# Optimization experiments

Measured on AMD Instinct MI355X. Metric: run time of the kernel, lower is better.

The kernel has to match this reference:

```python
import jax, jax.numpy as jnp
import numpy as np

B, S, H, NH = 2, 2048, 2048, 16
HD = H // NH

def setup_inputs() -> dict:
    key = jax.random.key(0)
    ks = jax.random.split(key, 6)
    scale = 1.0 / np.sqrt(H)
    return {
        "x": jax.random.normal(ks[0], (B, S, H), dtype=jnp.float32),
        "Wq": jax.random.normal(ks[1], (H, H), dtype=jnp.float32) * scale,
        "Wk": jax.random.normal(ks[2], (H, H), dtype=jnp.float32) * scale,
        "Wv": jax.random.normal(ks[3], (H, H), dtype=jnp.float32) * scale,
        "Wo": jax.random.normal(ks[4], (H, H), dtype=jnp.float32) * scale,
        "bo": jax.random.normal(ks[5], (H,), dtype=jnp.float32) * 0.01,
    }

def reference(x, Wq, Wk, Wv, Wo, bo):
    # nn.Linear convention: y = x @ W.T (W is [out, in])
    q = (x @ Wq.T).reshape(B, S, NH, HD).transpose(0, 2, 1, 3)  # [B,NH,S,HD]
    k = (x @ Wk.T).reshape(B, S, NH, HD).transpose(0, 2, 1, 3)
    v = (x @ Wv.T).reshape(B, S, NH, HD).transpose(0, 2, 1, 3)
    scale = jnp.asarray(HD, x.dtype) ** -0.5
    scores = jnp.einsum('bhqd,bhkd->bhqk', q, k) * scale  # [B,NH,S,S]
    attn = jax.nn.softmax(scores, axis=-1)
    out = jnp.einsum('bhqk,bhkd->bhqd', attn, v)  # [B,NH,S,HD]
    out = out.transpose(0, 2, 1, 3).reshape(B, S, H)
    return out @ Wo.T + bo
```

## Files before the change

### kernel.cpp

```cpp
#include <hip/hip_runtime.h>
#include <hip/hip_bf16.h>
#include <stdint.h>

#define S_LEN 2048
#define NHEADS 16
#define HDIM 128
#define H_TOT 2048
#define BATCH 2
#define M_TOK 4096
#define KDIM 2048

typedef __attribute__((ext_vector_type(8))) short bf16x8;
typedef __attribute__((ext_vector_type(4))) float f32x4;
typedef __attribute__((ext_vector_type(16))) float f32x16;

__device__ inline ushort bf16rn(float f) {
  union { float f; uint32_t u; } x; x.f = f;
  uint32_t r = x.u + 0x7FFF + ((x.u >> 16) & 1);
  return (ushort)(r >> 16);
}

__global__ __launch_bounds__(256) void cvt_bf16_kernel(const float* __restrict__ in,
                                                       ushort* __restrict__ out, int n4) {
  int i = blockIdx.x * blockDim.x + threadIdx.x;
  int stride = gridDim.x * blockDim.x;
  for (; i < n4; i += stride) {
    float4 v = reinterpret_cast<const float4*>(in)[i];
    ushort4 o;
    o.x = bf16rn(v.x); o.y = bf16rn(v.y); o.z = bf16rn(v.z); o.w = bf16rn(v.w);
    reinterpret_cast<ushort4*>(out)[i] = o;
  }
}

template<int MODE>
__global__ __launch_bounds__(256) void gemm_nt(const ushort* __restrict__ A,
                                               const ushort* __restrict__ Bw,
                                               void* __restrict__ Cout,
                                               const float* __restrict__ bias,
                                               float scale) {
  __shared__ ushort As[128 * 32];
  __shared__ ushort Bs[128 * 32];
  const int K = KDIM;
  int tid = threadIdx.x;
  int wave = tid >> 6, lane = tid & 63;
  int bm = blockIdx.y * 128, bn = blockIdx.x * 128;
  int wr = wave >> 1, wc = wave & 1;

  f32x4 acc[4][4];
#pragma unroll
  for (int i = 0; i < 4; i++)
#pragma unroll
    for (int j = 0; j < 4; j++) acc[i][j] = (f32x4){0.f, 0.f, 0.f, 0.f};

  int r0 = wave * 32 + (lane >> 2);
  int c8 = (lane & 3) * 8;
  const ushort* gA0 = A + (size_t)(bm + r0) * K + c8;
  const ushort* gA1 = gA0 + 16 * (size_t)K;
  const ushort* gB0 = Bw + (size_t)(bn + r0) * K + c8;
  const ushort* gB1 = gB0 + 16 * (size_t)K;
  ushort* lA0 = As + (wave * 2 + 0) * 512;
  ushort* lA1 = As + (wave * 2 + 1) * 512;
  ushort* lB0 = Bs + (wave * 2 + 0) * 512;
  ushort* lB1 = Bs + (wave * 2 + 1) * 512;

  int aoff = (wr * 64 + (lane & 15)) * 32 + (lane >> 4) * 8;
  int boff = (wc * 64 + (lane & 15)) * 32 + (lane >> 4) * 8;

  for (int kt = 0; kt < K; kt += 32) {
    __builtin_amdgcn_global_load_lds((const __attribute__((address_space(1))) void*)gA0,
                                     (__attribute__((address_space(3))) void*)lA0, 16, 0, 0);
    __builtin_amdgcn_global_load_lds((const __attribute__((address_space(1))) void*)gA1,
                                     (__attribute__((address_space(3))) void*)lA1, 16, 0, 0);
    __builtin_amdgcn_global_load_lds((const __attribute__((address_space(1))) void*)gB0,
                                     (__attribute__((address_space(3))) void*)lB0, 16, 0, 0);
    __builtin_amdgcn_global_load_lds((const __attribute__((address_space(1))) void*)gB1,
                                     (__attribute__((address_space(3))) void*)lB1, 16, 0, 0);
    __syncthreads();

    bf16x8 af[4], bfm[4];
#pragma unroll
    for (int i = 0; i < 4; i++) af[i] = *reinterpret_cast<const bf16x8*>(&As[aoff + i * 512]);
#pragma unroll
    for (int j = 0; j < 4; j++) bfm[j] = *reinterpret_cast<const bf16x8*>(&Bs[boff + j * 512]);
#pragma unroll
    for (int i = 0; i < 4; i++)
#pragma unroll
      for (int j = 0; j < 4; j++)
        acc[i][j] = __builtin_amdgcn_mfma_f32_16x16x32_bf16(af[i], bfm[j], acc[i][j], 0, 0, 0);
    __syncthreads();

    gA0 += 32; gA1 += 32; gB0 += 32; gB1 += 32;
  }

  int rbase = bm + wr * 64 + (lane >> 4) * 4;
  int cbase = bn + wc * 64 + (lane & 15);
  if (MODE == 2) {
    float* Cf = (float*)Cout;
#pragma unroll
    for (int j = 0; j < 4; j++) {
      int n = cbase + j * 16;
      float bv = bias[n];
#pragma unroll
      for (int i = 0; i < 4; i++)
#pragma unroll
        for (int q = 0; q < 4; q++) {
          int m = rbase + i * 16 + q;
          Cf[(size_t)m * H_TOT + n] = acc[i][j][q] + bv;
        }
    }
  } else {
    ushort* Cb = (ushort*)Cout;
#pragma unroll
    for (int j = 0; j < 4; j++) {
      int n = cbase + j * 16;
      int h = n >> 7, d = n & 127;
#pragma unroll
      for (int i = 0; i < 4; i++)
#pragma unroll
        for (int q = 0; q < 4; q++) {
          int m = rbase + i * 16 + q;
          int b = m >> 11, s = m & 2047;
          int bh = b * NHEADS + h;
          size_t idx;
          if (MODE == 0) {
            idx = (((size_t)(bh * 64 + (s >> 5)) * 8 + (d >> 4)) * 64 +
                   ((d >> 3) & 1) * 32 + (s & 31)) * 8 + (d & 7);
          } else {
            int r = s & 15;
            int e = (r & 3) | ((r >> 1) & 4);
            int hi = (r >> 2) & 1;
            idx = (((size_t)(bh * 64 + (s >> 5)) * 8 + ((s >> 4) & 1) * 4 + (d >> 5)) * 64 +
                   hi * 32 + (d & 31)) * 8 + e;
          }
          Cb[idx] = bf16rn(acc[i][j][q] * scale);
        }
    }
  }
}

__global__ __launch_bounds__(256) void attn_kernel(const ushort* __restrict__ Qf,
                                                   const ushort* __restrict__ Kf,
                                                   const ushort* __restrict__ Vf,
                                                   ushort* __restrict__ Ob) {
  __shared__ __attribute__((aligned(16))) ushort KV[2][8192];
  __shared__ float lsinv[4][32];
  int lane = threadIdx.x & 63, wave = threadIdx.x >> 6;
  int hi = lane >> 5;

  int bid = blockIdx.x;
  int swz = (bid & 7) * 64 + (bid >> 3);
  int bh = swz >> 4, qt = swz & 15;
  int b = bh >> 4, h = bh & 15;
  int qrow0 = qt * 128 + wave * 32;

  const bf16x8* Qv = reinterpret_cast<const bf16x8*>(Qf) +
                     ((size_t)(bh * 64 + qt * 4 + wave) * 8) * 64 + lane;
  bf16x8 qf[8];
#pragma unroll
  for (int kc = 0; kc < 8; kc++) qf[kc] = Qv[kc * 64];

  f32x16 oacc[4];
#pragma unroll
  for (int d32 = 0; d32 < 4; d32++)
#pragma unroll
    for (int r = 0; r < 16; r++) oacc[d32][r] = 0.f;
  float lsum = 0.f;

  const ushort* Kbase = Kf;
  const ushort* Vbase = Vf;
  int laneoff = lane * 8;

#define STAGE(kt, bufsel)                                                                  \
  {                                                                                        \
    size_t gchunk = ((size_t)(bh * 64 + (kt))) * 8;                                        \
    _Pragma("unroll")                                                                      \
    for (int i = 0; i < 4; i++) {                                                          \
      int cc = wave * 4 + i;                                                               \
      const ushort* src = (cc < 8) ? (Kbase + (gchunk + cc) * 512 + laneoff)               \
                                   : (Vbase + (gchunk + (cc - 8)) * 512 + laneoff);        \
      __builtin_amdgcn_global_load_lds((const __attribute__((address_space(1))) void*)src, \
                                       (__attribute__((address_space(3))) void*)           \
                                           (&KV[bufsel][cc * 512]),                        \
                                       16, 0, 0);                                          \
    }                                                                                      \
  }

  STAGE(0, 0);
  asm volatile("s_waitcnt vmcnt(0)" ::: "memory");
  __syncthreads();

  const int NT = S_LEN / 32;
  for (int t = 0; t < NT; t++) {
    if (t + 1 < NT) STAGE(t + 1, (t + 1) & 1);
    const ushort* lb = &KV[t & 1][0];

    f32x16 S;
#pragma unroll
    for (int r = 0; r < 16; r++) S[r] = 0.f;
    __builtin_amdgcn_s_setprio(1);
#pragma unroll
    for (int kc = 0; kc < 8; kc++) {
      bf16x8 kfr = *reinterpret_cast<const bf16x8*>(&lb[kc * 512 + laneoff]);
      S = __builtin_amdgcn_mfma_f32_32x32x16_bf16(kfr, qf[kc], S, 0, 0, 0);
    }
    __builtin_amdgcn_s_setprio(0);

    float p[16];
#pragma unroll
    for (int r = 0; r < 16; r++) {
      p[r] = exp2f(S[r]);
      lsum += p[r];
    }
    union { bf16x8 v; uint32_t u[4]; } pa0, pa1;
#pragma unroll
    for (int j = 0; j < 4; j++) {
      uint32_t w0, w1;
      asm("v_cvt_pk_bf16_f32 %0, %1, %2" : "=v"(w0) : "v"(p[2 * j]), "v"(p[2 * j + 1]));
      asm("v_cvt_pk_bf16_f32 %0, %1, %2" : "=v"(w1) : "v"(p[8 + 2 * j]), "v"(p[9 + 2 * j]));
      pa0.u[j] = w0;
      pa1.u[j] = w1;
    }

    __builtin_amdgcn_s_setprio(1);
#pragma unroll
    for (int d32 = 0; d32 < 4; d32++) {
      bf16x8 v0 = *reinterpret_cast<const bf16x8*>(&lb[4096 + (0 + d32) * 512 + laneoff]);
      bf16x8 v1 = *reinterpret_cast<const bf16x8*>(&lb[4096 + (4 + d32) * 512 + laneoff]);
      oacc[d32] = __builtin_amdgcn_mfma_f32_32x32x16_bf16(pa0.v, v0, oacc[d32], 0, 0, 0);
      oacc[d32] = __builtin_amdgcn_mfma_f32_32x32x16_bf16(pa1.v, v1, oacc[d32], 0, 0, 0);
    }
    __builtin_amdgcn_s_setprio(0);

    asm volatile("s_waitcnt vmcnt(0)" ::: "memory");
    __syncthreads();
  }

  float total = lsum + __shfl_xor(lsum, 32);
  if (lane < 32) lsinv[wave][lane] = 1.0f / total;
  __syncthreads();

  float ls[16];
#pragma unroll
  for (int r = 0; r < 16; r++) ls[r] = lsinv[wave][(r & 3) + 8 * (r >> 2) + 4 * hi];
#pragma unroll
  for (int d32 = 0; d32 < 4; d32++)
#pragma unroll
    for (int r = 0; r < 16; r++) {
      int row = (r & 3) + 8 * (r >> 2) + 4 * hi;
      size_t idx = ((size_t)(b * S_LEN + qrow0 + row)) * H_TOT + h * HDIM + d32 * 32 + (lane & 31);
      Ob[idx] = bf16rn(oacc[d32][r] * ls[r]);
    }
#undef STAGE
}

extern "C" void kernel_launch(void* const* d_in, const int* in_sizes, int n_in,
                              void* d_out, int out_size, void* d_ws, size_t ws_size,
                              hipStream_t stream) {
  const float* x  = (const float*)d_in[0];
  const float* Wq = (const float*)d_in[1];
  const float* Wk = (const float*)d_in[2];
  const float* Wv = (const float*)d_in[3];
  const float* Wo = (const float*)d_in[4];
  const float* bo = (const float*)d_in[5];
  float* out = (float*)d_out;

  char* w = (char*)d_ws;
  ushort* xb  = (ushort*)w; w += (size_t)M_TOK * KDIM * 2;
  ushort* Wqb = (ushort*)w; w += (size_t)KDIM * KDIM * 2;
  ushort* Wkb = (ushort*)w; w += (size_t)KDIM * KDIM * 2;
  ushort* Wvb = (ushort*)w; w += (size_t)KDIM * KDIM * 2;
  ushort* Wob = (ushort*)w; w += (size_t)KDIM * KDIM * 2;
  ushort* Qh  = (ushort*)w; w += (size_t)M_TOK * KDIM * 2;
  ushort* Kh  = (ushort*)w; w += (size_t)M_TOK * KDIM * 2;
  ushort* Vt  = (ushort*)w; w += (size_t)M_TOK * KDIM * 2;
  ushort* Ob  = (ushort*)w; w += (size_t)M_TOK * KDIM * 2;

  hipLaunchKernelGGL(cvt_bf16_kernel, dim3(2048), dim3(256), 0, stream, x,  xb,  M_TOK * KDIM / 4);
  hipLaunchKernelGGL(cvt_bf16_kernel, dim3(1024), dim3(256), 0, stream, Wq, Wqb, KDIM * KDIM / 4);
  hipLaunchKernelGGL(cvt_bf16_kernel, dim3(1024), dim3(256), 0, stream, Wk, Wkb, KDIM * KDIM / 4);
  hipLaunchKernelGGL(cvt_bf16_kernel, dim3(1024), dim3(256), 0, stream, Wv, Wvb, KDIM * KDIM / 4);
  hipLaunchKernelGGL(cvt_bf16_kernel, dim3(1024), dim3(256), 0, stream, Wo, Wob, KDIM * KDIM / 4);

  const float sl = 0.08838834764831845f * 1.4426950408889634f;
  dim3 g(H_TOT / 128, M_TOK / 128), blk(256);
  hipLaunchKernelGGL((gemm_nt<0>), g, blk, 0, stream, xb, Wqb, (void*)Qh, (const float*)nullptr, sl);
  hipLaunchKernelGGL((gemm_nt<0>), g, blk, 0, stream, xb, Wkb, (void*)Kh, (const float*)nullptr, 1.0f);
  hipLaunchKernelGGL((gemm_nt<1>), g, blk, 0, stream, xb, Wvb, (void*)Vt, (const float*)nullptr, 1.0f);

  hipLaunchKernelGGL(attn_kernel, dim3(512), blk, 0, stream, Qh, Kh, Vt, Ob);

  hipLaunchKernelGGL((gemm_nt<2>), g, blk, 0, stream, Ob, Wob, (void*)out, bo, 1.0f);
}
```

Before: 311.2 us.

## Software-pipeline attention PV, halve attention block size, swizzle GEMM grid, batch weight casts

The attention kernel now uses 2-wave blocks over 64 query rows, so twice as many blocks are launched. Each iteration issues the previous tile's PV MFMAs alongside the current QK MFMAs, with V fragments and P held in registers and ping-ponged between two sets. The GEMMs switch to a 1D grid with an XCD-aware tile swizzle, and the four weight conversions are merged into one launch. Together these aim for better MFMA/softmax overlap, more blocks per CU, better L2 locality and fewer launches. The cost is higher register pressure, and each K/V tile is now loaded by twice as many blocks.

```diff
diff --git a/kernel.cpp b/kernel.cpp
--- a/kernel.cpp
+++ b/kernel.cpp
@@ -29,6 +29,28 @@
     ushort4 o;
     o.x = bf16rn(v.x); o.y = bf16rn(v.y); o.z = bf16rn(v.z); o.w = bf16rn(v.w);
     reinterpret_cast<ushort4*>(out)[i] = o;
+  }
+}
+
+__global__ __launch_bounds__(256) void cvt4_bf16_kernel(const float* __restrict__ w0,
+                                                        const float* __restrict__ w1,
+                                                        const float* __restrict__ w2,
+                                                        const float* __restrict__ w3,
+                                                        ushort* __restrict__ o0,
+                                                        ushort* __restrict__ o1,
+                                                        ushort* __restrict__ o2,
+                                                        ushort* __restrict__ o3) {
+  const int N4 = KDIM * KDIM / 4;
+  int i = blockIdx.x * blockDim.x + threadIdx.x;
+  int stride = gridDim.x * blockDim.x;
+  for (; i < 4 * N4; i += stride) {
+    int seg = i >> 20, off = i & (N4 - 1);
+    const float* in = (seg == 0) ? w0 : (seg == 1) ? w1 : (seg == 2) ? w2 : w3;
+    ushort* out = (seg == 0) ? o0 : (seg == 1) ? o1 : (seg == 2) ? o2 : o3;
+    float4 v = reinterpret_cast<const float4*>(in)[off];
+    ushort4 o;
+    o.x = bf16rn(v.x); o.y = bf16rn(v.y); o.z = bf16rn(v.z); o.w = bf16rn(v.w);
+    reinterpret_cast<ushort4*>(out)[off] = o;
   }
 }
 
@@ -43,7 +65,11 @@
   const int K = KDIM;
   int tid = threadIdx.x;
   int wave = tid >> 6, lane = tid & 63;
-  int bm = blockIdx.y * 128, bn = blockIdx.x * 128;
+  int bid = blockIdx.x;
+  int c = bid & 7, ii = bid >> 3;
+  int bx = (c & 1) * 8 + (ii & 7);
+  int by = (c >> 1) * 8 + (ii >> 3);
+  int bm = by * 128, bn = bx * 128;
   int wr = wave >> 1, wc = wave & 1;
 
   f32x4 acc[4][4];
@@ -138,23 +164,23 @@
   }
 }
 
-__global__ __launch_bounds__(256) void attn_kernel(const ushort* __restrict__ Qf,
+__global__ __launch_bounds__(128) void attn_kernel(const ushort* __restrict__ Qf,
                                                    const ushort* __restrict__ Kf,
                                                    const ushort* __restrict__ Vf,
                                                    ushort* __restrict__ Ob) {
   __shared__ __attribute__((aligned(16))) ushort KV[2][8192];
-  __shared__ float lsinv[4][32];
+  __shared__ float lsinv[2][32];
   int lane = threadIdx.x & 63, wave = threadIdx.x >> 6;
   int hi = lane >> 5;
 
   int bid = blockIdx.x;
-  int swz = (bid & 7) * 64 + (bid >> 3);
-  int bh = swz >> 4, qt = swz & 15;
+  int swz = (bid & 7) * 128 + (bid >> 3);
+  int bh = swz >> 5, qt = swz & 31;
   int b = bh >> 4, h = bh & 15;
-  int qrow0 = qt * 128 + wave * 32;
+  int qrow0 = qt * 64 + wave * 32;
 
   const bf16x8* Qv = reinterpret_cast<const bf16x8*>(Qf) +
-                     ((size_t)(bh * 64 + qt * 4 + wave) * 8) * 64 + lane;
+                     ((size_t)(bh * 64 + qt * 2 + wave) * 8) * 64 + lane;
   bf16x8 qf[8];
 #pragma unroll
   for (int kc = 0; kc < 8; kc++) qf[kc] = Qv[kc * 64];
@@ -165,74 +191,73 @@
 #pragma unroll
     for (int r = 0; r < 16; r++) oacc[d32][r] = 0.f;
   float lsum = 0.f;
-
-  const ushort* Kbase = Kf;
-  const ushort* Vbase = Vf;
   int laneoff = lane * 8;
-
-#define STAGE(kt, bufsel)                                                                  \
-  {                                                                                        \
-    size_t gchunk = ((size_t)(bh * 64 + (kt))) * 8;                                        \
-    _Pragma("unroll")                                                                      \
-    for (int i = 0; i < 4; i++) {                                                          \
-      int cc = wave * 4 + i;                                                               \
-      const ushort* src = (cc < 8) ? (Kbase + (gchunk + cc) * 512 + laneoff)               \
-                                   : (Vbase + (gchunk + (cc - 8)) * 512 + laneoff);        \
-      __builtin_amdgcn_global_load_lds((const __attribute__((address_space(1))) void*)src, \
-                                       (__attribute__((address_space(3))) void*)           \
-                                           (&KV[bufsel][cc * 512]),                        \
-                                       16, 0, 0);                                          \
-    }                                                                                      \
-  }
+  const ushort* sbase = wave ? Vf : Kf;
+
+#define STAGE(kt, bufsel)                                                                   \
+  {                                                                                         \
+    size_t gc = ((size_t)(bh * 64 + (kt))) * 8;                                             \
+    _Pragma("unroll") for (int i_ = 0; i_ < 8; i_++) {                                      \
+      __builtin_amdgcn_global_load_lds(                                                     \
+          (const __attribute__((address_space(1))) void*)(sbase + (gc + i_) * 512 + laneoff),\
+          (__attribute__((address_space(3))) void*)(&KV[bufsel][(wave * 8 + i_) * 512]),    \
+          16, 0, 0);                                                                        \
+    }                                                                                       \
+  }
+
+  union pu { bf16x8 v; uint32_t u[4]; };
+  pu paA0, paA1, paB0, paB1;
+  bf16x8 vrA[8], vrB[8];
+  const bf16x8 bz = {0, 0, 0, 0, 0, 0, 0, 0};
+#pragma unroll
+  for (int j = 0; j < 4; j++) { paA0.u[j] = 0; paA1.u[j] = 0; }
+#pragma unroll
+  for (int i = 0; i < 8; i++) vrA[i] = bz;
 
   STAGE(0, 0);
   asm volatile("s_waitcnt vmcnt(0)" ::: "memory");
   __syncthreads();
 
   const int NT = S_LEN / 32;
-  for (int t = 0; t < NT; t++) {
-    if (t + 1 < NT) STAGE(t + 1, (t + 1) & 1);
-    const ushort* lb = &KV[t & 1][0];
-
-    f32x16 S;
-#pragma unroll
-    for (int r = 0; r < 16; r++) S[r] = 0.f;
-    __builtin_amdgcn_s_setprio(1);
-#pragma unroll
-    for (int kc = 0; kc < 8; kc++) {
-      bf16x8 kfr = *reinterpret_cast<const bf16x8*>(&lb[kc * 512 + laneoff]);
-      S = __builtin_amdgcn_mfma_f32_32x32x16_bf16(kfr, qf[kc], S, 0, 0, 0);
-    }
-    __builtin_amdgcn_s_setprio(0);
-
-    float p[16];
-#pragma unroll
-    for (int r = 0; r < 16; r++) {
-      p[r] = exp2f(S[r]);
-      lsum += p[r];
-    }
-    union { bf16x8 v; uint32_t u[4]; } pa0, pa1;
-#pragma unroll
-    for (int j = 0; j < 4; j++) {
-      uint32_t w0, w1;
-      asm("v_cvt_pk_bf16_f32 %0, %1, %2" : "=v"(w0) : "v"(p[2 * j]), "v"(p[2 * j + 1]));
-      asm("v_cvt_pk_bf16_f32 %0, %1, %2" : "=v"(w1) : "v"(p[8 + 2 * j]), "v"(p[9 + 2 * j]));
-      pa0.u[j] = w0;
-      pa1.u[j] = w1;
-    }
-
-    __builtin_amdgcn_s_setprio(1);
-#pragma unroll
-    for (int d32 = 0; d32 < 4; d32++) {
-      bf16x8 v0 = *reinterpret_cast<const bf16x8*>(&lb[4096 + (0 + d32) * 512 + laneoff]);
-      bf16x8 v1 = *reinterpret_cast<const bf16x8*>(&lb[4096 + (4 + d32) * 512 + laneoff]);
-      oacc[d32] = __builtin_amdgcn_mfma_f32_32x32x16_bf16(pa0.v, v0, oacc[d32], 0, 0, 0);
-      oacc[d32] = __builtin_amdgcn_mfma_f32_32x32x16_bf16(pa1.v, v1, oacc[d32], 0, 0, 0);
-    }
-    __builtin_amdgcn_s_setprio(0);
-
-    asm volatile("s_waitcnt vmcnt(0)" ::: "memory");
-    __syncthreads();
+
+#define BODY(T, PI0, PI1, VI, PO0, PO1, VO)                                                 \
+  {                                                                                         \
+    if ((T) + 1 < NT) STAGE((T) + 1, ((T) + 1) & 1);                                        \
+    const ushort* lb = &KV[(T) & 1][0];                                                     \
+    f32x16 S;                                                                               \
+    _Pragma("unroll") for (int r = 0; r < 16; r++) S[r] = 0.f;                              \
+    __builtin_amdgcn_s_setprio(1);                                                          \
+    _Pragma("unroll") for (int kc = 0; kc < 8; kc++) {                                      \
+      bf16x8 kfr = *reinterpret_cast<const bf16x8*>(&lb[kc * 512 + laneoff]);               \
+      S = __builtin_amdgcn_mfma_f32_32x32x16_bf16(kfr, qf[kc], S, 0, 0, 0);                 \
+    }                                                                                       \
+    _Pragma("unroll") for (int d32 = 0; d32 < 4; d32++) {                                   \
+      oacc[d32] = __builtin_amdgcn_mfma_f32_32x32x16_bf16(PI0.v, VI[d32], oacc[d32], 0, 0, 0); \
+      oacc[d32] = __builtin_amdgcn_mfma_f32_32x32x16_bf16(PI1.v, VI[4 + d32], oacc[d32], 0, 0, 0); \
+    }                                                                                       \
+    __builtin_amdgcn_s_setprio(0);                                                          \
+    float p_[16];                                                                           \
+    _Pragma("unroll") for (int r = 0; r < 16; r++) { p_[r] = exp2f(S[r]); lsum += p_[r]; }  \
+    _Pragma("unroll") for (int j = 0; j < 4; j++) {                                         \
+      uint32_t w0_, w1_;                                                                    \
+      asm("v_cvt_pk_bf16_f32 %0, %1, %2" : "=v"(w0_) : "v"(p_[2 * j]), "v"(p_[2 * j + 1])); \
+      asm("v_cvt_pk_bf16_f32 %0, %1, %2" : "=v"(w1_) : "v"(p_[8 + 2 * j]), "v"(p_[9 + 2 * j])); \
+      PO0.u[j] = w0_; PO1.u[j] = w1_;                                                       \
+    }                                                                                       \
+    _Pragma("unroll") for (int i_ = 0; i_ < 8; i_++)                                        \
+      VO[i_] = *reinterpret_cast<const bf16x8*>(&lb[4096 + i_ * 512 + laneoff]);            \
+    asm volatile("s_waitcnt vmcnt(0)" ::: "memory");                                        \
+    __syncthreads();                                                                        \
+  }
+
+  for (int t = 0; t < NT; t += 2) {
+    BODY(t,     paA0, paA1, vrA, paB0, paB1, vrB);
+    BODY(t + 1, paB0, paB1, vrB, paA0, paA1, vrA);
+  }
+#pragma unroll
+  for (int d32 = 0; d32 < 4; d32++) {
+    oacc[d32] = __builtin_amdgcn_mfma_f32_32x32x16_bf16(paA0.v, vrA[d32], oacc[d32], 0, 0, 0);
+    oacc[d32] = __builtin_amdgcn_mfma_f32_32x32x16_bf16(paA1.v, vrA[4 + d32], oacc[d32], 0, 0, 0);
   }
 
   float total = lsum + __shfl_xor(lsum, 32);
@@ -250,6 +275,7 @@
       size_t idx = ((size_t)(b * S_LEN + qrow0 + row)) * H_TOT + h * HDIM + d32 * 32 + (lane & 31);
       Ob[idx] = bf16rn(oacc[d32][r] * ls[r]);
     }
+#undef BODY
 #undef STAGE
 }
 
@@ -275,19 +301,17 @@
   ushort* Vt  = (ushort*)w; w += (size_t)M_TOK * KDIM * 2;
   ushort* Ob  = (ushort*)w; w += (size_t)M_TOK * KDIM * 2;
 
-  hipLaunchKernelGGL(cvt_bf16_kernel, dim3(2048), dim3(256), 0, stream, x,  xb,  M_TOK * KDIM / 4);
-  hipLaunchKernelGGL(cvt_bf16_kernel, dim3(1024), dim3(256), 0, stream, Wq, Wqb, KDIM * KDIM / 4);
-  hipLaunchKernelGGL(cvt_bf16_kernel, dim3(1024), dim3(256), 0, stream, Wk, Wkb, KDIM * KDIM / 4);
-  hipLaunchKernelGGL(cvt_bf16_kernel, dim3(1024), dim3(256), 0, stream, Wv, Wvb, KDIM * KDIM / 4);
-  hipLaunchKernelGGL(cvt_bf16_kernel, dim3(1024), dim3(256), 0, stream, Wo, Wob, KDIM * KDIM / 4);
+  hipLaunchKernelGGL(cvt_bf16_kernel, dim3(2048), dim3(256), 0, stream, x, xb, M_TOK * KDIM / 4);
+  hipLaunchKernelGGL(cvt4_bf16_kernel, dim3(2048), dim3(256), 0, stream,
+                     Wq, Wk, Wv, Wo, Wqb, Wkb, Wvb, Wob);
 
   const float sl = 0.08838834764831845f * 1.4426950408889634f;
-  dim3 g(H_TOT / 128, M_TOK / 128), blk(256);
+  dim3 g(512), blk(256);
   hipLaunchKernelGGL((gemm_nt<0>), g, blk, 0, stream, xb, Wqb, (void*)Qh, (const float*)nullptr, sl);
   hipLaunchKernelGGL((gemm_nt<0>), g, blk, 0, stream, xb, Wkb, (void*)Kh, (const float*)nullptr, 1.0f);
   hipLaunchKernelGGL((gemm_nt<1>), g, blk, 0, stream, xb, Wvb, (void*)Vt, (const float*)nullptr, 1.0f);
 
-  hipLaunchKernelGGL(attn_kernel, dim3(512), blk, 0, stream, Qh, Kh, Vt, Ob);
+  hipLaunchKernelGGL(attn_kernel, dim3(1024), dim3(128), 0, stream, Qh, Kh, Vt, Ob);
 
   hipLaunchKernelGGL((gemm_nt<2>), g, blk, 0, stream, Ob, Wob, (void*)out, bo, 1.0f);
 }
```

Measured after the change: 301.7 us. 1.03x faster.
